# Optimization experiments

Hardware: AMD Instinct MI355X
Metric: run time of the kernel (lower is better)

Reference implementation:

```python
import jax, jax.numpy as jnp
import numpy as np
import math

B, S, D, H, L = 4, 2048, 512, 8, 2
HD = D // H
NG = (3, 4, 5)
V = 30000          # n_gram_vocab_size
BASE = 31          # rolling hash base
NPATCH = 16
PLEN = S // NPATCH


def _ln(x, w, b, eps):
    m = x.mean(-1, keepdims=True)
    v = ((x - m) ** 2).mean(-1, keepdims=True)
    return (x - m) * jax.lax.rsqrt(v + eps) * w + b


def setup_inputs() -> dict:
    key = jax.random.key(0)
    ks = jax.random.split(key, 16)

    def nrm(i, shape, std=0.02):
        return jax.random.normal(ks[i], shape, dtype=jnp.float32) * std

    return {
        "byte_seq": jax.random.randint(ks[0], (B, S), 0, 256, dtype=jnp.int32),
        "patch_boundaries": jnp.arange(NPATCH + 1, dtype=jnp.int32) * PLEN,
        "byte_emb": nrm(1, (256, D), 1.0 / math.sqrt(D)),
        "ng_emb": nrm(2, (len(NG), V, D)),
        "tl_qkv_w": nrm(3, (L, 3 * D, D)),
        "tl_qkv_b": jnp.zeros((L, 3 * D), jnp.float32),
        "tl_out_w": nrm(4, (L, D, D)),
        "tl_out_b": jnp.zeros((L, D), jnp.float32),
        "tl_ln1_w": jnp.ones((L, D), jnp.float32),
        "tl_ln1_b": jnp.zeros((L, D), jnp.float32),
        "tl_ln2_w": jnp.ones((L, D), jnp.float32),
        "tl_ln2_b": jnp.zeros((L, D), jnp.float32),
        "tl_ff1_w": nrm(5, (L, 4 * D, D)),
        "tl_ff1_b": jnp.zeros((L, 4 * D), jnp.float32),
        "tl_ff2_w": nrm(6, (L, D, 4 * D)),
        "tl_ff2_b": jnp.zeros((L, D), jnp.float32),
        "ca_qkv_w": nrm(7, (3 * D, D)),
        "ca_qkv_b": jnp.zeros((3 * D,), jnp.float32),
        "ca_out_w": nrm(8, (D, D)),
        "ca_out_b": jnp.zeros((D,), jnp.float32),
        "ca_ln_w": jnp.ones((D,), jnp.float32),
        "ca_ln_b": jnp.zeros((D,), jnp.float32),
        "norm_w": jnp.ones((D,), jnp.float32),
        "norm_b": jnp.zeros((D,), jnp.float32),
    }


def _forward(byte_seq, patch_boundaries, byte_emb, ng_emb,
             tl_qkv_w, tl_qkv_b, tl_out_w, tl_out_b,
             tl_ln1_w, tl_ln1_b, tl_ln2_w, tl_ln2_b,
             tl_ff1_w, tl_ff1_b, tl_ff2_w, tl_ff2_b,
             ca_qkv_w, ca_qkv_b, ca_out_w, ca_out_b, ca_ln_w, ca_ln_b,
             norm_w, norm_b):
    x = byte_emb[byte_seq]                                  # [B,S,D]

    # n-gram rolling hash == polynomial hash mod V; computed in parallel
    # as windowed dot products with modular base powers (exact same values
    # as the sequential rolling-update loop in the torch code).
    ng_scale = 1.0 / (len(NG) + 1)
    for idx, n in enumerate(NG):
        powers = jnp.array([pow(BASE, n - 1 - i, V) for i in range(n)],
                           dtype=byte_seq.dtype)
        windows = jnp.stack([byte_seq[:, j:S - n + 1 + j] for j in range(n)],
                            axis=-1)                        # [B,S-n+1,n]
        h = (windows * powers).sum(-1) % V                   # [B,S-n+1]
        x = x.at[:, n - 1:].add(ng_emb[idx][h] * ng_scale)

    scale = 1.0 / math.sqrt(HD)
    neg = jnp.where(jnp.triu(jnp.ones((S, S), dtype=bool), 1),
                    -jnp.inf, 0.0).astype(x.dtype)           # causal additive mask

    # post-norm TransformerEncoderLayer (relu activation, dropout=0/eval)
    for l in range(L):
        qkv = x @ tl_qkv_w[l].T + tl_qkv_b[l]                # [B,S,3D]
        q, k, v = jnp.split(qkv, 3, axis=-1)
        q = q.reshape(B, S, H, HD).transpose(0, 2, 1, 3)
        k = k.reshape(B, S, H, HD).transpose(0, 2, 1, 3)
        v = v.reshape(B, S, H, HD).transpose(0, 2, 1, 3)
        scores = jnp.einsum('bhqd,bhkd->bhqk', q, k) * scale + neg
        a = jax.nn.softmax(scores, axis=-1)
        o = jnp.einsum('bhqk,bhkd->bhqd', a, v).transpose(0, 2, 1, 3).reshape(B, S, D)
        o = o @ tl_out_w[l].T + tl_out_b[l]
        x = _ln(x + o, tl_ln1_w[l], tl_ln1_b[l], 1e-5)
        ff = jax.nn.relu(x @ tl_ff1_w[l].T + tl_ff1_b[l]) @ tl_ff2_w[l].T + tl_ff2_b[l]
        x = _ln(x + ff, tl_ln2_w[l], tl_ln2_b[l], 1e-5)

    # uniform patch boundaries -> vectorized patch cross-attention
    npatch = patch_boundaries.shape[0] - 1
    plen = S // npatch
    xp = x.reshape(B, npatch, plen, D)
    query = xp.mean(axis=2)                                  # [B,P,D]
    qn = _ln(query, ca_ln_w, ca_ln_b, 1e-6)
    kvn = _ln(xp, ca_ln_w, ca_ln_b, 1e-6)
    wq, wk, wv = jnp.split(ca_qkv_w, 3, axis=0)
    bq, bk, bv = jnp.split(ca_qkv_b, 3)
    q = (qn @ wq.T + bq).reshape(B, npatch, H, HD)
    k = (kvn @ wk.T + bk).reshape(B, npatch, plen, H, HD)
    v = (kvn @ wv.T + bv).reshape(B, npatch, plen, H, HD)
    s = jnp.einsum('bphd,bplhd->bphl', q, k) * scale
    a = jax.nn.softmax(s, axis=-1)
    o = jnp.einsum('bphl,bplhd->bphd', a, v).reshape(B, npatch, D)
    patches = query + (o @ ca_out_w.T + ca_out_b)

    return _ln(x, norm_w, norm_b, 1e-6), _ln(patches, norm_w, norm_b, 1e-6)


def reference(byte_seq, patch_boundaries, byte_emb, ng_emb,
              tl_qkv_w, tl_qkv_b, tl_out_w, tl_out_b,
              tl_ln1_w, tl_ln1_b, tl_ln2_w, tl_ln2_b,
              tl_ff1_w, tl_ff1_b, tl_ff2_w, tl_ff2_b,
              ca_qkv_w, ca_qkv_b, ca_out_w, ca_out_b, ca_ln_w, ca_ln_b,
              norm_w, norm_b):
    return _forward(byte_seq, patch_boundaries, byte_emb, ng_emb,
                    tl_qkv_w, tl_qkv_b, tl_out_w, tl_out_b,
                    tl_ln1_w, tl_ln1_b, tl_ln2_w, tl_ln2_b,
                    tl_ff1_w, tl_ff1_b, tl_ff2_w, tl_ff2_b,
                    ca_qkv_w, ca_qkv_b, ca_out_w, ca_out_b, ca_ln_w, ca_ln_b,
                    norm_w, norm_b)
```

## Files before the change

### kernel.cpp

```cpp
#include <hip/hip_runtime.h>
#include <hip/hip_bf16.h>

#define B_ 4
#define S_ 2048
#define D_ 512
#define H_ 8
#define HD_ 64
#define L_ 2
#define V_ 30000
#define NPATCH_ 16
#define PLEN_ 128

typedef short bf16x8 __attribute__((ext_vector_type(8)));
typedef float f32x4 __attribute__((ext_vector_type(4)));

__device__ __forceinline__ unsigned short f2bf(float f) {
    unsigned u = __float_as_uint(f);
    return (unsigned short)((u + 0x7FFFu + ((u >> 16) & 1u)) >> 16);
}

#define C0_ (2*1536*512/4)
#define C1_ (2*512*512/4)
#define C2_ (2*2048*512/4)
#define C3_ (2*512*2048/4)
#define C4_ (1024*512/4)
__global__ __launch_bounds__(256) void cast5_kernel(
    const float* __restrict__ s0, const float* __restrict__ s1,
    const float* __restrict__ s2, const float* __restrict__ s3,
    const float* __restrict__ s4,
    unsigned short* __restrict__ d0, unsigned short* __restrict__ d1,
    unsigned short* __restrict__ d2, unsigned short* __restrict__ d3,
    unsigned short* __restrict__ d4)
{
    int i = blockIdx.x * 256 + threadIdx.x;
    const float* s; unsigned short* d;
    if      (i < C0_)                  { s = s0; d = d0; }
    else if ((i -= C0_) < C1_)         { s = s1; d = d1; }
    else if ((i -= C1_) < C2_)         { s = s2; d = d2; }
    else if ((i -= C2_) < C3_)         { s = s3; d = d3; }
    else if ((i -= C3_) < C4_)         { s = s4; d = d4; }
    else return;
    const float4 v = *reinterpret_cast<const float4*>(s + (size_t)i * 4);
    ushort4 o;
    o.x = f2bf(v.x); o.y = f2bf(v.y); o.z = f2bf(v.z); o.w = f2bf(v.w);
    *reinterpret_cast<ushort4*>(d + (size_t)i * 4) = o;
}

__global__ __launch_bounds__(128) void embed_ngram_kernel(
    const int* __restrict__ bytes, const float* __restrict__ byte_emb,
    const float* __restrict__ ng_emb, float* __restrict__ x,
    unsigned short* __restrict__ xb)
{
    const int bs = blockIdx.x;
    const int s  = bs % S_;
    const int b  = bs / S_;
    const int d  = threadIdx.x * 4;
    const int* brow = bytes + (size_t)b * S_;

    const int c = brow[s];
    float4 v = *reinterpret_cast<const float4*>(byte_emb + (size_t)c * D_ + d);

    if (s >= 2) {
        int h = (brow[s-2]*961 + brow[s-1]*31 + brow[s]) % V_;
        const float4 g = *reinterpret_cast<const float4*>(ng_emb + ((size_t)0*V_ + h)*D_ + d);
        v.x += 0.25f*g.x; v.y += 0.25f*g.y; v.z += 0.25f*g.z; v.w += 0.25f*g.w;
    }
    if (s >= 3) {
        int h = (brow[s-3]*29791 + brow[s-2]*961 + brow[s-1]*31 + brow[s]) % V_;
        const float4 g = *reinterpret_cast<const float4*>(ng_emb + ((size_t)1*V_ + h)*D_ + d);
        v.x += 0.25f*g.x; v.y += 0.25f*g.y; v.z += 0.25f*g.z; v.w += 0.25f*g.w;
    }
    if (s >= 4) {
        int h = (brow[s-4]*23521 + brow[s-3]*29791 + brow[s-2]*961 + brow[s-1]*31 + brow[s]) % V_;
        const float4 g = *reinterpret_cast<const float4*>(ng_emb + ((size_t)2*V_ + h)*D_ + d);
        v.x += 0.25f*g.x; v.y += 0.25f*g.y; v.z += 0.25f*g.z; v.w += 0.25f*g.w;
    }
    *reinterpret_cast<float4*>(x + (size_t)bs * D_ + d) = v;
    ushort4 o;
    o.x = f2bf(v.x); o.y = f2bf(v.y); o.z = f2bf(v.z); o.w = f2bf(v.w);
    *reinterpret_cast<ushort4*>(xb + (size_t)bs * D_ + d) = o;
}

template<int DO_RELU, int BF16OUT, int BN>
__global__ __launch_bounds__(256) void mgemm_kernel(
    const unsigned short* __restrict__ Xb, const unsigned short* __restrict__ Wb,
    const float* __restrict__ bias, void* __restrict__ Yout,
    int M, int N, int K)
{
    constexpr int NT  = BN / 32;
    constexpr int NLB = BN / 32;
    __shared__ unsigned short As[128*64];
    __shared__ unsigned short Bs[BN*64];

    const int t    = threadIdx.x;
    const int lane = t & 63;
    const int w    = t >> 6;
    const int bm   = blockIdx.y * 128, bn = blockIdx.x * BN;
    const int l15  = lane & 15, lg = lane >> 4;
    const int wr   = w >> 1, wc = w & 1;

    int srow[4], scol[4];
#pragma unroll
    for (int i = 0; i < 4; ++i) {
        const int off = w*1024 + i*4096 + lane*16;
        srow[i] = off >> 7;
        scol[i] = ((off >> 4) & 7) ^ (srow[i] & 7);
    }

    f32x4 acc[4][NT];
#pragma unroll
    for (int mt = 0; mt < 4; ++mt)
#pragma unroll
        for (int nt = 0; nt < NT; ++nt) acc[mt][nt] = (f32x4){0.f,0.f,0.f,0.f};

    for (int kt = 0; kt < K; kt += 64) {
#pragma unroll
        for (int i = 0; i < 4; ++i) {
            const unsigned short* gA = Xb + (size_t)(bm + srow[i]) * K + kt + scol[i]*8;
            __builtin_amdgcn_global_load_lds(
                (const __attribute__((address_space(1))) void*)gA,
                (__attribute__((address_space(3))) void*)&As[w*512 + i*2048], 16, 0, 0);
        }
#pragma unroll
        for (int i = 0; i < NLB; ++i) {
            const unsigned short* gB = Wb + (size_t)(bn + srow[i]) * K + kt + scol[i]*8;
            __builtin_amdgcn_global_load_lds(
                (const __attribute__((address_space(1))) void*)gB,
                (__attribute__((address_space(3))) void*)&Bs[w*512 + i*2048], 16, 0, 0);
        }
        __syncthreads();

#pragma unroll
        for (int ks = 0; ks < 2; ++ks) {
            const int c16 = (ks*4 + lg) ^ (l15 & 7);
            bf16x8 a[4], b[NT];
#pragma unroll
            for (int mt = 0; mt < 4; ++mt)
                a[mt] = *reinterpret_cast<const bf16x8*>(&As[(wr*64 + mt*16 + l15)*64 + c16*8]);
#pragma unroll
            for (int nt = 0; nt < NT; ++nt)
                b[nt] = *reinterpret_cast<const bf16x8*>(&Bs[(wc*(BN/2) + nt*16 + l15)*64 + c16*8]);
#pragma unroll
            for (int mt = 0; mt < 4; ++mt)
#pragma unroll
                for (int nt = 0; nt < NT; ++nt)
                    acc[mt][nt] = __builtin_amdgcn_mfma_f32_16x16x32_bf16(
                        a[mt], b[nt], acc[mt][nt], 0, 0, 0);
        }
        __syncthreads();
    }

    float bv[NT];
#pragma unroll
    for (int nt = 0; nt < NT; ++nt) bv[nt] = bias[bn + wc*(BN/2) + nt*16 + l15];

#pragma unroll
    for (int mt = 0; mt < 4; ++mt) {
#pragma unroll
        for (int nt = 0; nt < NT; ++nt) {
            const int n = bn + wc*(BN/2) + nt*16 + l15;
#pragma unroll
            for (int r = 0; r < 4; ++r) {
                const int m = bm + wr*64 + mt*16 + 4*lg + r;
                float v = acc[mt][nt][r] + bv[nt];
                if (DO_RELU) v = fmaxf(v, 0.f);
                if (BF16OUT)
                    ((unsigned short*)Yout)[(size_t)m * N + n] = f2bf(v);
                else
                    ((float*)Yout)[(size_t)m * N + n] = v;
            }
        }
    }
}

__global__ __launch_bounds__(256) void gemm_kernel(
    const float* __restrict__ X, const float* __restrict__ W,
    const float* __restrict__ bias, const float* __restrict__ resid,
    float* __restrict__ Y, int M, int N, int K, int do_relu)
{
    __shared__ float As[16][68];
    __shared__ float Bs[16][68];
    const int tid = threadIdx.x;
    const int bm = blockIdx.y * 64, bn = blockIdx.x * 64;
    const int ty = tid >> 4, tx = tid & 15;
    const int lrow = tid >> 2, lc4 = (tid & 3) * 4;

    float acc[4][4];
#pragma unroll
    for (int i = 0; i < 4; ++i)
#pragma unroll
        for (int j = 0; j < 4; ++j) acc[i][j] = 0.f;

    for (int k0 = 0; k0 < K; k0 += 16) {
        const float4 xv = *reinterpret_cast<const float4*>(X + (size_t)(bm + lrow) * K + k0 + lc4);
        const float4 wv = *reinterpret_cast<const float4*>(W + (size_t)(bn + lrow) * K + k0 + lc4);
        __syncthreads();
        As[lc4+0][lrow] = xv.x; As[lc4+1][lrow] = xv.y;
        As[lc4+2][lrow] = xv.z; As[lc4+3][lrow] = xv.w;
        Bs[lc4+0][lrow] = wv.x; Bs[lc4+1][lrow] = wv.y;
        Bs[lc4+2][lrow] = wv.z; Bs[lc4+3][lrow] = wv.w;
        __syncthreads();
#pragma unroll
        for (int kk = 0; kk < 16; ++kk) {
            float a0 = As[kk][ty*4+0], a1 = As[kk][ty*4+1], a2 = As[kk][ty*4+2], a3 = As[kk][ty*4+3];
            float b0 = Bs[kk][tx*4+0], b1 = Bs[kk][tx*4+1], b2 = Bs[kk][tx*4+2], b3 = Bs[kk][tx*4+3];
            acc[0][0] += a0*b0; acc[0][1] += a0*b1; acc[0][2] += a0*b2; acc[0][3] += a0*b3;
            acc[1][0] += a1*b0; acc[1][1] += a1*b1; acc[1][2] += a1*b2; acc[1][3] += a1*b3;
            acc[2][0] += a2*b0; acc[2][1] += a2*b1; acc[2][2] += a2*b2; acc[2][3] += a2*b3;
            acc[3][0] += a3*b0; acc[3][1] += a3*b1; acc[3][2] += a3*b2; acc[3][3] += a3*b3;
        }
    }

#pragma unroll
    for (int i = 0; i < 4; ++i) {
        const int m = bm + ty*4 + i;
#pragma unroll
        for (int j = 0; j < 4; ++j) {
            const int n = bn + tx*4 + j;
            float v = acc[i][j] + bias[n];
            if (do_relu) v = fmaxf(v, 0.f);
            if (resid) v += resid[(size_t)m * N + n];
            Y[(size_t)m * N + n] = v;
        }
    }
}

__global__ __launch_bounds__(256) void attn_mfma_kernel(
    const unsigned short* __restrict__ qkvb, unsigned short* __restrict__ ob)
{
    __shared__ unsigned short Ks[128*72];
    __shared__ unsigned short Vt[64*136];
    __shared__ unsigned short Plds[4*16*136];

    const int t    = threadIdx.x;
    const int lane = t & 63;
    const int w    = t >> 6;
    const int qp   = blockIdx.x;
    const int bh   = blockIdx.y;
    const int h    = bh & 7;
    const int b    = bh >> 3;

    const unsigned short* base = qkvb + (size_t)b * S_ * 1536;
    const int l15 = lane & 15, lg = lane >> 4;
    const int skey = t >> 1;
    const int sd0  = (t & 1) * 32;
    const int scs  = (((skey >> 3) ^ ((t & 1) << 1)) << 3) + (skey & 7);
    unsigned short* pw_base = Plds + w*16*136;

    bf16x8 kr0, kr1, kr2, kr3, vr0, vr1, vr2, vr3;
#define LOADREG(KT) { \
        const unsigned short* p_ = base + (size_t)((KT) + skey) * 1536 + 512 + h*64 + sd0; \
        kr0 = *reinterpret_cast<const bf16x8*>(p_);       \
        kr1 = *reinterpret_cast<const bf16x8*>(p_ + 8);   \
        kr2 = *reinterpret_cast<const bf16x8*>(p_ + 16);  \
        kr3 = *reinterpret_cast<const bf16x8*>(p_ + 24);  \
        vr0 = *reinterpret_cast<const bf16x8*>(p_ + 512); \
        vr1 = *reinterpret_cast<const bf16x8*>(p_ + 520); \
        vr2 = *reinterpret_cast<const bf16x8*>(p_ + 528); \
        vr3 = *reinterpret_cast<const bf16x8*>(p_ + 536); }

    LOADREG(0);

#pragma unroll
    for (int half = 0; half < 2; ++half) {
        const int qb  = half ? (31 - qp) : qp;
        const int q0w = qb * 64 + w * 16;

        bf16x8 qf0, qf1;
        {
            const unsigned short* qr = base + (size_t)(q0w + l15) * 1536 + h*64 + lg*8;
            qf0 = *reinterpret_cast<const bf16x8*>(qr);
            qf1 = *reinterpret_cast<const bf16x8*>(qr + 32);
        }

        f32x4 oacc[4];
#pragma unroll
        for (int i = 0; i < 4; ++i) oacc[i] = (f32x4){0.f,0.f,0.f,0.f};
        float mrow[4] = {-INFINITY,-INFINITY,-INFINITY,-INFINITY};
        float lrow[4] = {0.f,0.f,0.f,0.f};

        const int ntiles = (qb + 2) >> 1;
        for (int tile = 0; tile < ntiles; ++tile) {
            const int kt = tile * 128;
            __syncthreads();
            *reinterpret_cast<bf16x8*>(&Ks[skey*72 + sd0])      = kr0;
            *reinterpret_cast<bf16x8*>(&Ks[skey*72 + sd0 + 8])  = kr1;
            *reinterpret_cast<bf16x8*>(&Ks[skey*72 + sd0 + 16]) = kr2;
            *reinterpret_cast<bf16x8*>(&Ks[skey*72 + sd0 + 24]) = kr3;
#pragma unroll
            for (int j = 0; j < 8; ++j) Vt[(sd0+j)*136    + scs] = (unsigned short)vr0[j];
#pragma unroll
            for (int j = 0; j < 8; ++j) Vt[(sd0+8+j)*136  + scs] = (unsigned short)vr1[j];
#pragma unroll
            for (int j = 0; j < 8; ++j) Vt[(sd0+16+j)*136 + scs] = (unsigned short)vr2[j];
#pragma unroll
            for (int j = 0; j < 8; ++j) Vt[(sd0+24+j)*136 + scs] = (unsigned short)vr3[j];
            __syncthreads();
            const int nkt = (tile + 1 < ntiles) ? (kt + 128) : 0;
            LOADREG(nkt);

            f32x4 sacc[8];
            __builtin_amdgcn_s_setprio(1);
#pragma unroll
            for (int kt16 = 0; kt16 < 8; ++kt16) {
                sacc[kt16] = (f32x4){0.f,0.f,0.f,0.f};
                const unsigned short* kp = &Ks[(kt16*16 + l15)*72 + lg*8];
                bf16x8 k0 = *reinterpret_cast<const bf16x8*>(kp);
                bf16x8 k1 = *reinterpret_cast<const bf16x8*>(kp + 32);
                sacc[kt16] = __builtin_amdgcn_mfma_f32_16x16x32_bf16(qf0, k0, sacc[kt16], 0, 0, 0);
                sacc[kt16] = __builtin_amdgcn_mfma_f32_16x16x32_bf16(qf1, k1, sacc[kt16], 0, 0, 0);
            }
            __builtin_amdgcn_s_setprio(0);

            const bool diag = (tile == ntiles - 1);
#pragma unroll
            for (int kt16 = 0; kt16 < 8; ++kt16) {
#pragma unroll
                for (int r = 0; r < 4; ++r) {
                    float s = sacc[kt16][r] * 0.125f;
                    if (diag) {
                        const int key = kt + kt16*16 + l15;
                        const int q   = q0w + 4*lg + r;
                        if (key > q) s = -INFINITY;
                    }
                    sacc[kt16][r] = s;
                }
            }
#pragma unroll
            for (int r = 0; r < 4; ++r) {
                float tm = fmaxf(
                    fmaxf(fmaxf(sacc[0][r], sacc[1][r]), fmaxf(sacc[2][r], sacc[3][r])),
                    fmaxf(fmaxf(sacc[4][r], sacc[5][r]), fmaxf(sacc[6][r], sacc[7][r])));
#pragma unroll
                for (int off = 8; off; off >>= 1) tm = fmaxf(tm, __shfl_xor(tm, off, 64));
                const float nm = fmaxf(mrow[r], tm);
                const float al = __expf(mrow[r] - nm);
                mrow[r] = nm;
                float ps = 0.f;
#pragma unroll
                for (int kt16 = 0; kt16 < 8; ++kt16) {
                    const float p = __expf(sacc[kt16][r] - nm);
                    ps += p;
                    pw_base[(4*lg + r)*136 + kt16*16 + l15] = f2bf(p);
                }
#pragma unroll
                for (int off = 8; off; off >>= 1) ps += __shfl_xor(ps, off, 64);
                lrow[r] = lrow[r]*al + ps;
#pragma unroll
                for (int dt = 0; dt < 4; ++dt) oacc[dt][r] *= al;
            }

            const unsigned short* pr = &pw_base[l15*136 + lg*8];
            bf16x8 pa0 = *reinterpret_cast<const bf16x8*>(pr);
            bf16x8 pa1 = *reinterpret_cast<const bf16x8*>(pr + 32);
            bf16x8 pa2 = *reinterpret_cast<const bf16x8*>(pr + 64);
            bf16x8 pa3 = *reinterpret_cast<const bf16x8*>(pr + 96);
            __builtin_amdgcn_s_setprio(1);
#pragma unroll
            for (int dt = 0; dt < 4; ++dt) {
                const unsigned short* vrow = &Vt[(dt*16 + l15)*136];
                bf16x8 v0 = *reinterpret_cast<const bf16x8*>(&vrow[(( 0 + lg) ^ (dt & 2))*8]);
                bf16x8 v1 = *reinterpret_cast<const bf16x8*>(&vrow[(( 4 + lg) ^ (dt & 2))*8]);
                bf16x8 v2 = *reinterpret_cast<const bf16x8*>(&vrow[(( 8 + lg) ^ (dt & 2))*8]);
                bf16x8 v3 = *reinterpret_cast<const bf16x8*>(&vrow[((12 + lg) ^ (dt & 2))*8]);
                oacc[dt] = __builtin_amdgcn_mfma_f32_16x16x32_bf16(pa0, v0, oacc[dt], 0, 0, 0);
                oacc[dt] = __builtin_amdgcn_mfma_f32_16x16x32_bf16(pa1, v1, oacc[dt], 0, 0, 0);
                oacc[dt] = __builtin_amdgcn_mfma_f32_16x16x32_bf16(pa2, v2, oacc[dt], 0, 0, 0);
                oacc[dt] = __builtin_amdgcn_mfma_f32_16x16x32_bf16(pa3, v3, oacc[dt], 0, 0, 0);
            }
            __builtin_amdgcn_s_setprio(0);
        }

#pragma unroll
        for (int dt = 0; dt < 4; ++dt) {
#pragma unroll
            for (int r = 0; r < 4; ++r) {
                const int q = q0w + 4*lg + r;
                ob[((size_t)b*S_ + q)*D_ + h*64 + dt*16 + l15] = f2bf(oacc[dt][r] / lrow[r]);
            }
        }
    }
#undef LOADREG
}

__global__ __launch_bounds__(256) void ln_kernel(
    float* __restrict__ dst, unsigned short* __restrict__ dst2,
    const float* __restrict__ src, const float* __restrict__ add,
    const float* __restrict__ w, const float* __restrict__ b, float eps)
{
    const int row = blockIdx.x, tid = threadIdx.x;
    const int lane = tid & 63, wave = tid >> 6;
    float2 v = *reinterpret_cast<const float2*>(src + (size_t)row * D_ + tid*2);
    if (add) {
        float2 a = *reinterpret_cast<const float2*>(add + (size_t)row * D_ + tid*2);
        v.x += a.x; v.y += a.y;
    }
    __shared__ float red[8];
    float s = v.x + v.y;
#pragma unroll
    for (int off = 32; off; off >>= 1) s += __shfl_xor(s, off, 64);
    if (lane == 0) red[wave] = s;
    __syncthreads();
    const float mean = (red[0]+red[1]+red[2]+red[3]) * (1.f/D_);
    const float d0 = v.x - mean, d1 = v.y - mean;
    float sq = d0*d0 + d1*d1;
#pragma unroll
    for (int off = 32; off; off >>= 1) sq += __shfl_xor(sq, off, 64);
    if (lane == 0) red[4+wave] = sq;
    __syncthreads();
    const float var = (red[4]+red[5]+red[6]+red[7]) * (1.f/D_);
    const float inv = rsqrtf(var + eps);
    const float o0 = d0*inv*w[tid*2] + b[tid*2];
    const float o1 = d1*inv*w[tid*2+1] + b[tid*2+1];
    *reinterpret_cast<float2*>(dst + (size_t)row * D_ + tid*2) = make_float2(o0, o1);
    if (dst2) {
        ushort2 u; u.x = f2bf(o0); u.y = f2bf(o1);
        *reinterpret_cast<ushort2*>(dst2 + (size_t)row * D_ + tid*2) = u;
    }
}

__global__ __launch_bounds__(256) void meanpool_kernel(
    const float* __restrict__ x, float* __restrict__ query)
{
    const int bp = blockIdx.x;
    const int d = threadIdx.x * 2;
    const float* base = x + (size_t)bp * PLEN_ * D_ + d;
    float s0 = 0.f, s1 = 0.f;
    for (int l = 0; l < PLEN_; ++l) {
        float2 v = *reinterpret_cast<const float2*>(base + (size_t)l * D_);
        s0 += v.x; s1 += v.y;
    }
    query[(size_t)bp*D_ + d]     = s0 * (1.f/PLEN_);
    query[(size_t)bp*D_ + d + 1] = s1 * (1.f/PLEN_);
}

__global__ __launch_bounds__(256) void patch_attn_kernel(
    const float* __restrict__ qbuf, const float* __restrict__ kv,
    float* __restrict__ o)
{
    const int wid  = blockIdx.x * 4 + (threadIdx.x >> 6);
    const int lane = threadIdx.x & 63;
    const int h  = wid % H_;
    const int bp = wid / H_;
    const float qv = qbuf[(size_t)bp*D_ + h*HD_ + lane] * 0.125f;
    const float* base = kv + (size_t)bp * PLEN_ * 1024 + h*HD_;

    float m = -INFINITY, l = 0.f, acc = 0.f;
    for (int t = 0; t < PLEN_; ++t) {
        const float* row = base + (size_t)t * 1024;
        float s = qv * row[lane];
#pragma unroll
        for (int off = 32; off; off >>= 1) s += __shfl_xor(s, off, 64);
        const float vv = row[512 + lane];
        const float nm = fmaxf(m, s);
        const float al = __expf(m - nm);
        const float p  = __expf(s - nm);
        l = l * al + p;
        acc = acc * al + p * vv;
        m = nm;
    }
    o[(size_t)bp*D_ + h*HD_ + lane] = acc / l;
}

extern "C" void kernel_launch(void* const* d_in, const int* in_sizes, int n_in,
                              void* d_out, int out_size, void* d_ws, size_t ws_size,
                              hipStream_t stream)
{
    const int*   byte_seq = (const int*)d_in[0];
    const float* byte_emb = (const float*)d_in[2];
    const float* ng_emb   = (const float*)d_in[3];
    const float* qkv_w = (const float*)d_in[4];
    const float* qkv_b = (const float*)d_in[5];
    const float* out_w = (const float*)d_in[6];
    const float* out_b = (const float*)d_in[7];
    const float* ln1_w = (const float*)d_in[8];
    const float* ln1_b = (const float*)d_in[9];
    const float* ln2_w = (const float*)d_in[10];
    const float* ln2_b = (const float*)d_in[11];
    const float* ff1_w = (const float*)d_in[12];
    const float* ff1_b = (const float*)d_in[13];
    const float* ff2_w = (const float*)d_in[14];
    const float* ff2_b = (const float*)d_in[15];
    const float* ca_qkv_w = (const float*)d_in[16];
    const float* ca_qkv_b = (const float*)d_in[17];
    const float* ca_out_w = (const float*)d_in[18];
    const float* ca_out_b = (const float*)d_in[19];
    const float* ca_ln_w  = (const float*)d_in[20];
    const float* ca_ln_b  = (const float*)d_in[21];
    const float* norm_w   = (const float*)d_in[22];
    const float* norm_b   = (const float*)d_in[23];
    float* out = (float*)d_out;

    char* ws = (char*)d_ws;
    const size_t MB = 1024*1024;
    float*          x     = (float*)(ws);
    char*           bufA  = ws + 16*MB;
    float*          bufB  = (float*)(ws + 48*MB);
    unsigned short* ob    = (unsigned short*)(ws + 64*MB);
    unsigned short* xb    = (unsigned short*)(ws + 72*MB);
    unsigned short* qkvw_b = (unsigned short*)(ws + 80*MB);
    unsigned short* outw_b = (unsigned short*)(ws + 83*MB);
    unsigned short* ff1w_b = (unsigned short*)(ws + 84*MB);
    unsigned short* ff2w_b = (unsigned short*)(ws + 88*MB);
    unsigned short* kvw_b  = (unsigned short*)(ws + 92*MB);
    float* query   = (float*)(ws + 93*MB);
    float* qn      = query + 64*512;
    float* qsm     = qn + 64*512;
    float* oca     = qsm + 64*512;
    float* patches = oca + 64*512;

    unsigned short* qkvb = (unsigned short*)bufA;
    unsigned short* ff1b = (unsigned short*)bufA;
    float*          kvf  = (float*)bufA;

    const int M = B_ * S_;

    cast5_kernel<<<(C0_+C1_+C2_+C3_+C4_+255)/256, 256, 0, stream>>>(
        qkv_w, out_w, ff1_w, ff2_w, ca_qkv_w + 512*512,
        qkvw_b, outw_b, ff1w_b, ff2w_b, kvw_b);

    embed_ngram_kernel<<<M, 128, 0, stream>>>(byte_seq, byte_emb, ng_emb, x, xb);

    for (int l = 0; l < L_; ++l) {
        mgemm_kernel<0,1,128><<<dim3(1536/128, M/128), 256, 0, stream>>>(
            xb, qkvw_b + (size_t)l*1536*D_, qkv_b + l*1536, qkvb, M, 1536, D_);
        attn_mfma_kernel<<<dim3(S_/128, B_*H_), 256, 0, stream>>>(qkvb, ob);
        mgemm_kernel<0,0,64><<<dim3(D_/64, M/128), 256, 0, stream>>>(
            ob, outw_b + (size_t)l*D_*D_, out_b + l*D_, bufB, M, D_, D_);
        ln_kernel<<<M, 256, 0, stream>>>(x, xb, x, bufB, ln1_w + l*D_, ln1_b + l*D_, 1e-5f);
        mgemm_kernel<1,1,128><<<dim3(2048/128, M/128), 256, 0, stream>>>(
            xb, ff1w_b + (size_t)l*2048*D_, ff1_b + l*2048, ff1b, M, 2048, D_);
        mgemm_kernel<0,0,64><<<dim3(D_/64, M/128), 256, 0, stream>>>(
            ff1b, ff2w_b + (size_t)l*D_*2048, ff2_b + l*D_, bufB, M, D_, 2048);
        ln_kernel<<<M, 256, 0, stream>>>(x, xb, x, bufB, ln2_w + l*D_, ln2_b + l*D_, 1e-5f);
    }

    meanpool_kernel<<<B_*NPATCH_, 256, 0, stream>>>(x, query);
    ln_kernel<<<B_*NPATCH_, 256, 0, stream>>>(qn, nullptr, query, nullptr, ca_ln_w, ca_ln_b, 1e-6f);
    ln_kernel<<<M, 256, 0, stream>>>(bufB, xb, x, nullptr, ca_ln_w, ca_ln_b, 1e-6f);
    mgemm_kernel<0,0,128><<<dim3(1024/128, M/128), 256, 0, stream>>>(
        xb, kvw_b, ca_qkv_b + 512, kvf, M, 1024, D_);
    gemm_kernel<<<dim3(D_/64, 1), 256, 0, stream>>>(
        qn, ca_qkv_w, ca_qkv_b, nullptr, qsm, 64, D_, D_, 0);
    patch_attn_kernel<<<B_*NPATCH_*H_/4, 256, 0, stream>>>(qsm, kvf, oca);
    gemm_kernel<<<dim3(D_/64, 1), 256, 0, stream>>>(
        oca, ca_out_w, ca_out_b, query, patches, 64, D_, D_, 0);

    ln_kernel<<<M, 256, 0, stream>>>(out, nullptr, x, nullptr, norm_w, norm_b, 1e-6f);
    ln_kernel<<<B_*NPATCH_, 256, 0, stream>>>(
        out + (size_t)M*D_, nullptr, patches, nullptr, norm_w, norm_b, 1e-6f);
}
```

Measured before the change: 568.0 us.

## Fuse patch cross-attention tail into one kernel and swizzle GEMM block order

Replaces the meanpool, query LN, two small fp32 GEMMs, patch attention and final patch LN with a single per-patch kernel that keeps intermediates in shared memory. The ca-LN pass over all bytes also stops writing its unused fp32 output. Separately, the MFMA GEMM remaps block IDs with a stride-8 swizzle, intended to improve cache locality. The fused kernel runs only 64 blocks with serial per-thread dot products over D, which may leave the tail latency-bound.

```diff
diff --git a/kernel.cpp b/kernel.cpp
--- a/kernel.cpp
+++ b/kernel.cpp
@@ -95,7 +95,13 @@
     const int t    = threadIdx.x;
     const int lane = t & 63;
     const int w    = t >> 6;
-    const int bm   = blockIdx.y * 128, bn = blockIdx.x * BN;
+
+    const int nwg = gridDim.x * gridDim.y;
+    const int bid = blockIdx.y * gridDim.x + blockIdx.x;
+    const int swz = (bid & 7) * (nwg >> 3) + (bid >> 3);
+    const int bx  = swz % gridDim.x, by = swz / gridDim.x;
+
+    const int bm   = by * 128, bn = bx * BN;
     const int l15  = lane & 15, lg = lane >> 4;
     const int wr   = w >> 1, wc = w & 1;
 
@@ -169,58 +175,6 @@
                 else
                     ((float*)Yout)[(size_t)m * N + n] = v;
             }
-        }
-    }
-}
-
-__global__ __launch_bounds__(256) void gemm_kernel(
-    const float* __restrict__ X, const float* __restrict__ W,
-    const float* __restrict__ bias, const float* __restrict__ resid,
-    float* __restrict__ Y, int M, int N, int K, int do_relu)
-{
-    __shared__ float As[16][68];
-    __shared__ float Bs[16][68];
-    const int tid = threadIdx.x;
-    const int bm = blockIdx.y * 64, bn = blockIdx.x * 64;
-    const int ty = tid >> 4, tx = tid & 15;
-    const int lrow = tid >> 2, lc4 = (tid & 3) * 4;
-
-    float acc[4][4];
-#pragma unroll
-    for (int i = 0; i < 4; ++i)
-#pragma unroll
-        for (int j = 0; j < 4; ++j) acc[i][j] = 0.f;
-
-    for (int k0 = 0; k0 < K; k0 += 16) {
-        const float4 xv = *reinterpret_cast<const float4*>(X + (size_t)(bm + lrow) * K + k0 + lc4);
-        const float4 wv = *reinterpret_cast<const float4*>(W + (size_t)(bn + lrow) * K + k0 + lc4);
-        __syncthreads();
-        As[lc4+0][lrow] = xv.x; As[lc4+1][lrow] = xv.y;
-        As[lc4+2][lrow] = xv.z; As[lc4+3][lrow] = xv.w;
-        Bs[lc4+0][lrow] = wv.x; Bs[lc4+1][lrow] = wv.y;
-        Bs[lc4+2][lrow] = wv.z; Bs[lc4+3][lrow] = wv.w;
-        __syncthreads();
-#pragma unroll
-        for (int kk = 0; kk < 16; ++kk) {
-            float a0 = As[kk][ty*4+0], a1 = As[kk][ty*4+1], a2 = As[kk][ty*4+2], a3 = As[kk][ty*4+3];
-            float b0 = Bs[kk][tx*4+0], b1 = Bs[kk][tx*4+1], b2 = Bs[kk][tx*4+2], b3 = Bs[kk][tx*4+3];
-            acc[0][0] += a0*b0; acc[0][1] += a0*b1; acc[0][2] += a0*b2; acc[0][3] += a0*b3;
-            acc[1][0] += a1*b0; acc[1][1] += a1*b1; acc[1][2] += a1*b2; acc[1][3] += a1*b3;
-            acc[2][0] += a2*b0; acc[2][1] += a2*b1; acc[2][2] += a2*b2; acc[2][3] += a2*b3;
-            acc[3][0] += a3*b0; acc[3][1] += a3*b1; acc[3][2] += a3*b2; acc[3][3] += a3*b3;
-        }
-    }
-
-#pragma unroll
-    for (int i = 0; i < 4; ++i) {
-        const int m = bm + ty*4 + i;
-#pragma unroll
-        for (int j = 0; j < 4; ++j) {
-            const int n = bn + tx*4 + j;
-            float v = acc[i][j] + bias[n];
-            if (do_relu) v = fmaxf(v, 0.f);
-            if (resid) v += resid[(size_t)m * N + n];
-            Y[(size_t)m * N + n] = v;
         }
     }
 }
@@ -412,54 +366,190 @@
     const float inv = rsqrtf(var + eps);
     const float o0 = d0*inv*w[tid*2] + b[tid*2];
     const float o1 = d1*inv*w[tid*2+1] + b[tid*2+1];
-    *reinterpret_cast<float2*>(dst + (size_t)row * D_ + tid*2) = make_float2(o0, o1);
+    if (dst)
+        *reinterpret_cast<float2*>(dst + (size_t)row * D_ + tid*2) = make_float2(o0, o1);
     if (dst2) {
         ushort2 u; u.x = f2bf(o0); u.y = f2bf(o1);
         *reinterpret_cast<ushort2*>(dst2 + (size_t)row * D_ + tid*2) = u;
     }
 }
 
-__global__ __launch_bounds__(256) void meanpool_kernel(
-    const float* __restrict__ x, float* __restrict__ query)
+__global__ __launch_bounds__(256) void patch_tail_kernel(
+    const float* __restrict__ x, const float* __restrict__ kvf,
+    const float* __restrict__ ca_qkv_w, const float* __restrict__ ca_qkv_b,
+    const float* __restrict__ ca_out_w, const float* __restrict__ ca_out_b,
+    const float* __restrict__ ca_ln_w, const float* __restrict__ ca_ln_b,
+    const float* __restrict__ norm_w, const float* __restrict__ norm_b,
+    float* __restrict__ out)
 {
+    __shared__ float query[512];
+    __shared__ float qs[512];
+    __shared__ float ps[8*128];
+    __shared__ float os[512];
+    __shared__ float red[64];
+    __shared__ float mred[8], sred[8];
+
+    const int t  = threadIdx.x;
     const int bp = blockIdx.x;
-    const int d = threadIdx.x * 2;
-    const float* base = x + (size_t)bp * PLEN_ * D_ + d;
-    float s0 = 0.f, s1 = 0.f;
-    for (int l = 0; l < PLEN_; ++l) {
-        float2 v = *reinterpret_cast<const float2*>(base + (size_t)l * D_);
-        s0 += v.x; s1 += v.y;
-    }
-    query[(size_t)bp*D_ + d]     = s0 * (1.f/PLEN_);
-    query[(size_t)bp*D_ + d + 1] = s1 * (1.f/PLEN_);
-}
-
-__global__ __launch_bounds__(256) void patch_attn_kernel(
-    const float* __restrict__ qbuf, const float* __restrict__ kv,
-    float* __restrict__ o)
-{
-    const int wid  = blockIdx.x * 4 + (threadIdx.x >> 6);
-    const int lane = threadIdx.x & 63;
-    const int h  = wid % H_;
-    const int bp = wid / H_;
-    const float qv = qbuf[(size_t)bp*D_ + h*HD_ + lane] * 0.125f;
-    const float* base = kv + (size_t)bp * PLEN_ * 1024 + h*HD_;
-
-    float m = -INFINITY, l = 0.f, acc = 0.f;
-    for (int t = 0; t < PLEN_; ++t) {
-        const float* row = base + (size_t)t * 1024;
-        float s = qv * row[lane];
+    const int d0 = t * 2;
+    const int lane = t & 63, wave = t >> 6;
+
+    {
+        const float* base = x + (size_t)bp * PLEN_ * D_ + d0;
+        float s0 = 0.f, s1 = 0.f;
+        for (int l = 0; l < PLEN_; ++l) {
+            float2 v = *reinterpret_cast<const float2*>(base + (size_t)l * D_);
+            s0 += v.x; s1 += v.y;
+        }
+        query[d0] = s0 * (1.f/PLEN_);
+        query[d0+1] = s1 * (1.f/PLEN_);
+    }
+    __syncthreads();
+
+    float qv0 = query[d0], qv1 = query[d0+1];
+    {
+        float s = qv0 + qv1;
 #pragma unroll
         for (int off = 32; off; off >>= 1) s += __shfl_xor(s, off, 64);
-        const float vv = row[512 + lane];
-        const float nm = fmaxf(m, s);
-        const float al = __expf(m - nm);
-        const float p  = __expf(s - nm);
-        l = l * al + p;
-        acc = acc * al + p * vv;
-        m = nm;
-    }
-    o[(size_t)bp*D_ + h*HD_ + lane] = acc / l;
+        if (lane == 0) red[wave] = s;
+        __syncthreads();
+        const float mean = (red[0]+red[1]+red[2]+red[3]) * (1.f/D_);
+        const float e0 = qv0 - mean, e1 = qv1 - mean;
+        float sq = e0*e0 + e1*e1;
+#pragma unroll
+        for (int off = 32; off; off >>= 1) sq += __shfl_xor(sq, off, 64);
+        if (lane == 0) red[4+wave] = sq;
+        __syncthreads();
+        const float var = (red[4]+red[5]+red[6]+red[7]) * (1.f/D_);
+        const float inv = rsqrtf(var + 1e-6f);
+        qs[d0]   = e0*inv*ca_ln_w[d0]   + ca_ln_b[d0];
+        qs[d0+1] = e1*inv*ca_ln_w[d0+1] + ca_ln_b[d0+1];
+    }
+    __syncthreads();
+
+    float qp0, qp1;
+    {
+        const float* w0 = ca_qkv_w + (size_t)d0 * D_;
+        float a0 = ca_qkv_b[d0], a1 = ca_qkv_b[d0+1];
+        for (int e = 0; e < D_; e += 4) {
+            const float4 qn4 = *reinterpret_cast<const float4*>(&qs[e]);
+            const float4 wa = *reinterpret_cast<const float4*>(w0 + e);
+            const float4 wb = *reinterpret_cast<const float4*>(w0 + D_ + e);
+            a0 += qn4.x*wa.x + qn4.y*wa.y + qn4.z*wa.z + qn4.w*wa.w;
+            a1 += qn4.x*wb.x + qn4.y*wb.y + qn4.z*wb.z + qn4.w*wb.w;
+        }
+        qp0 = a0 * 0.125f; qp1 = a1 * 0.125f;
+    }
+    __syncthreads();
+    qs[d0] = qp0; qs[d0+1] = qp1;
+    __syncthreads();
+
+    {
+        const int h = t >> 5, c = t & 31;
+        const float* qh = &qs[h*64];
+#pragma unroll
+        for (int j = 0; j < 4; ++j) {
+            const int l = c*4 + j;
+            const float* krow = kvf + ((size_t)bp*PLEN_ + l)*1024 + h*64;
+            float acc = 0.f;
+            for (int e = 0; e < 64; e += 4) {
+                const float4 qe = *reinterpret_cast<const float4*>(qh + e);
+                const float4 ke = *reinterpret_cast<const float4*>(krow + e);
+                acc += qe.x*ke.x + qe.y*ke.y + qe.z*ke.z + qe.w*ke.w;
+            }
+            ps[h*128 + l] = acc;
+        }
+    }
+    __syncthreads();
+
+    {
+        const int h = t >> 5, c = t & 31;
+        float m4 = fmaxf(fmaxf(ps[h*128+c*4], ps[h*128+c*4+1]),
+                         fmaxf(ps[h*128+c*4+2], ps[h*128+c*4+3]));
+        red[h*8 + (c>>2)] = 0.f;
+        __syncthreads();
+        float mt_ = m4;
+#pragma unroll
+        for (int off = 1; off < 4; off <<= 1) mt_ = fmaxf(mt_, __shfl_xor(mt_, off, 64));
+        if ((c & 3) == 0) red[h*8 + (c>>2)] = mt_;
+        __syncthreads();
+        if (t < 8) {
+            float m = red[t*8];
+#pragma unroll
+            for (int j = 1; j < 8; ++j) m = fmaxf(m, red[t*8+j]);
+            mred[t] = m;
+        }
+        __syncthreads();
+        const float mh = mred[h];
+        float ssum = 0.f;
+#pragma unroll
+        for (int j = 0; j < 4; ++j) {
+            const float p = __expf(ps[h*128 + c*4 + j] - mh);
+            ps[h*128 + c*4 + j] = p;
+            ssum += p;
+        }
+#pragma unroll
+        for (int off = 1; off < 4; off <<= 1) ssum += __shfl_xor(ssum, off, 64);
+        if ((c & 3) == 0) red[h*8 + (c>>2)] = ssum;
+        __syncthreads();
+        if (t < 8) {
+            float s = 0.f;
+#pragma unroll
+            for (int j = 0; j < 8; ++j) s += red[t*8+j];
+            sred[t] = 1.f / s;
+        }
+    }
+    __syncthreads();
+
+    {
+        const int h = t >> 5;
+        const float* vbase = kvf + (size_t)bp*PLEN_*1024 + 512 + d0;
+        float a0 = 0.f, a1 = 0.f;
+        const float* ph = &ps[h*128];
+        for (int l = 0; l < PLEN_; ++l) {
+            const float p = ph[l];
+            const float2 vv = *reinterpret_cast<const float2*>(vbase + (size_t)l*1024);
+            a0 += p * vv.x; a1 += p * vv.y;
+        }
+        os[d0]   = a0 * sred[h];
+        os[d0+1] = a1 * sred[h];
+    }
+    __syncthreads();
+
+    float r0, r1;
+    {
+        const float* w0 = ca_out_w + (size_t)d0 * D_;
+        float a0 = ca_out_b[d0], a1 = ca_out_b[d0+1];
+        for (int e = 0; e < D_; e += 4) {
+            const float4 oe = *reinterpret_cast<const float4*>(&os[e]);
+            const float4 wa = *reinterpret_cast<const float4*>(w0 + e);
+            const float4 wb = *reinterpret_cast<const float4*>(w0 + D_ + e);
+            a0 += oe.x*wa.x + oe.y*wa.y + oe.z*wa.z + oe.w*wa.w;
+            a1 += oe.x*wb.x + oe.y*wb.y + oe.z*wb.z + oe.w*wb.w;
+        }
+        r0 = query[d0] + a0;
+        r1 = query[d0+1] + a1;
+    }
+    {
+        float s = r0 + r1;
+#pragma unroll
+        for (int off = 32; off; off >>= 1) s += __shfl_xor(s, off, 64);
+        __syncthreads();
+        if (lane == 0) red[wave] = s;
+        __syncthreads();
+        const float mean = (red[0]+red[1]+red[2]+red[3]) * (1.f/D_);
+        const float e0 = r0 - mean, e1 = r1 - mean;
+        float sq = e0*e0 + e1*e1;
+#pragma unroll
+        for (int off = 32; off; off >>= 1) sq += __shfl_xor(sq, off, 64);
+        if (lane == 0) red[4+wave] = sq;
+        __syncthreads();
+        const float var = (red[4]+red[5]+red[6]+red[7]) * (1.f/D_);
+        const float inv = rsqrtf(var + 1e-6f);
+        float* orow = out + ((size_t)(B_*S_) + bp) * D_;
+        orow[d0]   = e0*inv*norm_w[d0]   + norm_b[d0];
+        orow[d0+1] = e1*inv*norm_w[d0+1] + norm_b[d0+1];
+    }
 }
 
 extern "C" void kernel_launch(void* const* d_in, const int* in_sizes, int n_in,
@@ -503,11 +593,6 @@
     unsigned short* ff1w_b = (unsigned short*)(ws + 84*MB);
     unsigned short* ff2w_b = (unsigned short*)(ws + 88*MB);
     unsigned short* kvw_b  = (unsigned short*)(ws + 92*MB);
-    float* query   = (float*)(ws + 93*MB);
-    float* qn      = query + 64*512;
-    float* qsm     = qn + 64*512;
-    float* oca     = qsm + 64*512;
-    float* patches = oca + 64*512;
 
     unsigned short* qkvb = (unsigned short*)bufA;
     unsigned short* ff1b = (unsigned short*)bufA;
@@ -535,18 +620,12 @@
         ln_kernel<<<M, 256, 0, stream>>>(x, xb, x, bufB, ln2_w + l*D_, ln2_b + l*D_, 1e-5f);
     }
 
-    meanpool_kernel<<<B_*NPATCH_, 256, 0, stream>>>(x, query);
-    ln_kernel<<<B_*NPATCH_, 256, 0, stream>>>(qn, nullptr, query, nullptr, ca_ln_w, ca_ln_b, 1e-6f);
-    ln_kernel<<<M, 256, 0, stream>>>(bufB, xb, x, nullptr, ca_ln_w, ca_ln_b, 1e-6f);
+    ln_kernel<<<M, 256, 0, stream>>>(nullptr, xb, x, nullptr, ca_ln_w, ca_ln_b, 1e-6f);
     mgemm_kernel<0,0,128><<<dim3(1024/128, M/128), 256, 0, stream>>>(
         xb, kvw_b, ca_qkv_b + 512, kvf, M, 1024, D_);
-    gemm_kernel<<<dim3(D_/64, 1), 256, 0, stream>>>(
-        qn, ca_qkv_w, ca_qkv_b, nullptr, qsm, 64, D_, D_, 0);
-    patch_attn_kernel<<<B_*NPATCH_*H_/4, 256, 0, stream>>>(qsm, kvf, oca);
-    gemm_kernel<<<dim3(D_/64, 1), 256, 0, stream>>>(
-        oca, ca_out_w, ca_out_b, query, patches, 64, D_, D_, 0);
+    patch_tail_kernel<<<B_*NPATCH_, 256, 0, stream>>>(
+        x, kvf, ca_qkv_w, ca_qkv_b, ca_out_w, ca_out_b,
+        ca_ln_w, ca_ln_b, norm_w, norm_b, out);
 
     ln_kernel<<<M, 256, 0, stream>>>(out, nullptr, x, nullptr, norm_w, norm_b, 1e-6f);
-    ln_kernel<<<B_*NPATCH_, 256, 0, stream>>>(
-        out + (size_t)M*D_, nullptr, patches, nullptr, norm_w, norm_b, 1e-6f);
-}
+}
```

Result: faster. 513.4 us (-9.6%).
